# Optimization experiments

Measured on AMD Instinct MI355X. Metric: run time of the kernel, lower is better.

The kernel has to match this reference:

```python
import jax, jax.numpy as jnp
import numpy as np

B, S, D, H, O = 256, 64, 256, 1024, 512
N_CELLS = 3


def setup_inputs() -> dict:
    key = jax.random.key(0)
    ks = jax.random.split(key, 16)

    def u(k, shape, fan):
        return (jax.random.uniform(k, shape, jnp.float32, -1.0, 1.0) / np.float32(np.sqrt(fan)))

    inp = {"inputs": jax.random.normal(ks[0], (B, S, D), jnp.float32)}
    in_dims = [D, H, H]
    i = 1
    for c in range(N_CELLS):
        inp[f"w_ih_{c}"] = u(ks[i], (3 * H, in_dims[c]), H); i += 1
        inp[f"w_hh_{c}"] = u(ks[i], (3 * H, H), H); i += 1
        inp[f"b_ih_{c}"] = u(ks[i], (3 * H,), H); i += 1
        inp[f"b_hh_{c}"] = u(ks[i], (3 * H,), H); i += 1
    inp["lin_w"] = u(ks[13], (S, H, O), H)   # per-step linear weights (same_linear=False)
    inp["lin_b"] = u(ks[14], (S, O), H)
    return inp


def _gru_cell(x, h, w_ih, w_hh, b_ih, b_hh):
    # PyTorch GRUCell gate order: r, z, n
    gi = x @ w_ih.T + b_ih          # [B, 3H]
    gh = h @ w_hh.T + b_hh          # [B, 3H]
    i_r, i_z, i_n = jnp.split(gi, 3, axis=-1)
    h_r, h_z, h_n = jnp.split(gh, 3, axis=-1)
    r = jax.nn.sigmoid(i_r + h_r)
    z = jax.nn.sigmoid(i_z + h_z)
    n = jnp.tanh(i_n + r * h_n)
    return (1.0 - z) * n + z * h


def reference(inputs, w_ih_0, w_hh_0, b_ih_0, b_hh_0,
              w_ih_1, w_hh_1, b_ih_1, b_hh_1,
              w_ih_2, w_hh_2, b_ih_2, b_hh_2,
              lin_w, lin_b):
    params = [(w_ih_0, w_hh_0, b_ih_0, b_hh_0),
              (w_ih_1, w_hh_1, b_ih_1, b_hh_1),
              (w_ih_2, w_hh_2, b_ih_2, b_hh_2)]
    batch = inputs.shape[0]
    hdim = w_hh_0.shape[1]

    def step(hs, xs):
        x_t, wL, bL = xs              # [B,D], [H,O], [O]
        new_hs = []
        cur = x_t
        for i, (wi, wh, bi, bh) in enumerate(params):
            h = _gru_cell(cur, hs[i], wi, wh, bi, bh)
            new_hs.append(h)
            cur = h
        out = cur @ wL + bL           # [B,O]
        return tuple(new_hs), out

    h0 = tuple(jnp.zeros((batch, hdim), inputs.dtype) for _ in range(N_CELLS))
    xs = (jnp.swapaxes(inputs, 0, 1), lin_w, lin_b)  # scan over seq dim
    hs, outs = jax.lax.scan(step, h0, xs)            # outs: [S,B,O]
    return (jnp.swapaxes(outs, 0, 1), hs[0], hs[1], hs[2])
```

## Files before the change

kernel.cpp:

```cpp
#include <hip/hip_runtime.h>
#include <hip/hip_bf16.h>
#include <stdint.h>

#define B_ 256
#define S_ 64
#define D_ 256
#define H_ 1024
#define O_ 512
#define G_ 3072
#define BH_ (B_ * H_)
#define RING_ 32

typedef unsigned short u16;
typedef __attribute__((ext_vector_type(8))) short bf16x8;
typedef __attribute__((ext_vector_type(4))) float f32x4;

#define MFMA16(a, b, c) __builtin_amdgcn_mfma_f32_16x16x32_bf16((a), (b), (c), 0, 0, 0)

__device__ __forceinline__ u16 f2b(float f) {
    union { float f; uint32_t u; } v; v.f = f;
    uint32_t u = v.u;
    return (u16)((u + 0x7fffu + ((u >> 16) & 1u)) >> 16);
}

__device__ __forceinline__ void gl_lds16(const u16* g, u16* l) {
    __builtin_amdgcn_global_load_lds(
        (const __attribute__((address_space(1))) unsigned int*)g,
        (__attribute__((address_space(3))) unsigned int*)l, 16, 0, 0);
}
__device__ __forceinline__ unsigned long long gld_sys(const u16* p) {
    unsigned long long v;
    asm volatile("global_load_dwordx2 %0, %1, off sc0 sc1"
                 : "=v"(v) : "v"(p) : "memory");
    return v;
}
__device__ __forceinline__ void gst_sys(u16* p, unsigned long long v) {
    asm volatile("global_store_dwordx2 %0, %1, off sc0 sc1"
                 :: "v"(p), "v"(v) : "memory");
}
__device__ __forceinline__ void waitflag(int* f, int n) {
    while (__hip_atomic_load(f, __ATOMIC_RELAXED, __HIP_MEMORY_SCOPE_SYSTEM) < n)
        __builtin_amdgcn_s_sleep(8);
    asm volatile("" ::: "memory");
}
__device__ __forceinline__ void postflag(int* f) {
    __hip_atomic_fetch_add(f, 1, __ATOMIC_RELAXED, __HIP_MEMORY_SCOPE_SYSTEM);
}


__global__ void k_conv(const float* __restrict__ s, u16* __restrict__ d, int n4) {
    int i = blockIdx.x * blockDim.x + threadIdx.x;
    int st = gridDim.x * blockDim.x;
    for (; i < n4; i += st) {
        float4 v = ((const float4*)s)[i];
        ushort4 o;
        o.x = f2b(v.x); o.y = f2b(v.y); o.z = f2b(v.z); o.w = f2b(v.w);
        ((ushort4*)d)[i] = o;
    }
}

__global__ __launch_bounds__(256) void k_twl(const float* __restrict__ w, u16* __restrict__ o) {
    __shared__ float tile[32][33];
    int bid = blockIdx.x;
    int t = bid >> 9;
    int rem = bid & 511;
    int j0 = (rem >> 4) << 5;
    int o0 = (rem & 15) << 5;
    int tx = threadIdx.x & 31, ty = threadIdx.x >> 5;
    const float* base = w + (size_t)t * (H_ * O_);
#pragma unroll
    for (int i = 0; i < 4; ++i) {
        int r = ty + (i << 3);
        tile[r][tx] = base[(size_t)(j0 + r) * O_ + o0 + tx];
    }
    __syncthreads();
    u16* ob = o + (size_t)t * (O_ * H_);
#pragma unroll
    for (int i = 0; i < 4; ++i) {
        int r = ty + (i << 3);
        ob[(size_t)(o0 + r) * H_ + j0 + tx] = f2b(tile[tx][r]);
    }
}


struct GruArgs {
    const u16* Xb;
    const u16 *Wi0, *Wh0, *Wi1, *Wh1, *Wi2, *Wh2;
    const float *bi0, *bh0, *bi1, *bh1, *bi2, *bh2;
    u16 *h0, *h1, *h2a;
    const u16* WLt;
    const float* lb;
    float* out;
    int* ready;
    int* consumed;
};

__global__ __launch_bounds__(512, 1) void k_gru(GruArgs p) {
    __shared__ u16 Wb[3][3][128 * 64];
    __shared__ u16 Ab[2][32 * 64];

    const int w = blockIdx.x;
    const int xcd = w & 7;
    const int slot = w >> 3;
    const int role = slot >> 3;
    const int sub = slot & 7;
    const int b0 = sub * 32;

    const int tid = threadIdx.x;
    const int wid = tid >> 6, lane = tid & 63;
    const int fr = lane & 15, kc = lane >> 4;

    const int arow = tid >> 4;
    const int acol = (tid & 15) << 2;
    const int adst = arow * 64 + ((((tid & 15) >> 1) ^ (arow & 7)) << 3) + ((tid & 1) << 2);

    int sw0 = ((kc ^ (fr & 7)) << 3);
    int sw1 = (((4 + kc) ^ (fr & 7)) << 3);

    int* ready = p.ready;
    int* consumed = p.consumed;

    if (role < 3) {
        const u16 *Wi, *Wh; const float *bi, *bh; int K0;
        if (role == 0)      { Wi = p.Wi0; Wh = p.Wh0; bi = p.bi0; bh = p.bh0; K0 = D_; }
        else if (role == 1) { Wi = p.Wi1; Wh = p.Wh1; bi = p.bi1; bh = p.bh1; K0 = H_; }
        else                { Wi = p.Wi2; Wh = p.Wh2; bi = p.bi2; bh = p.bh2; K0 = H_; }
        const int nXc = K0 >> 6;
        const int nC = nXc + 16;
        const int j0 = xcd * 128;
        const int jme = j0 + (wid << 4) + fr;
        const float b_r = bi[jme] + bh[jme];
        const float b_z = bi[H_ + jme] + bh[H_ + jme];
        const float b_i = bi[2 * H_ + jme];
        const float b_h = bh[2 * H_ + jme];

        const u16 *A0 = nullptr, *Ah = nullptr; int ld0 = H_;
        u16* hout = nullptr;

        f32x4 hcar[2] = {};

        auto LA = [&](int c) -> unsigned long long {
            const u16* s = (c < nXc) ? (A0 + (size_t)arow * ld0 + (c << 6) + acol)
                                     : (Ah + (size_t)arow * H_ + ((c - nXc) << 6) + acol);
            return gld_sys(s);
        };
        auto SW = [&](int c, int nb) {
            if (c < nXc) {
                int ko = c << 6;
#pragma unroll
                for (int hh = 0; hh < 2; ++hh) {
                    int ci = (hh << 9) + tid, jr = ci >> 3, c8 = ci & 7;
                    size_t ro = (size_t)(j0 + jr) * K0 + ko + ((c8 ^ (jr & 7)) << 3);
                    gl_lds16(Wi + ro,                       &Wb[nb][0][ci << 3]);
                    gl_lds16(Wi + (size_t)H_ * K0 + ro,     &Wb[nb][1][ci << 3]);
                    gl_lds16(Wi + (size_t)2 * H_ * K0 + ro, &Wb[nb][2][ci << 3]);
                }
            } else {
                int ko = (c - nXc) << 6;
#pragma unroll
                for (int hh = 0; hh < 2; ++hh) {
                    int ci = (hh << 9) + tid, jr = ci >> 3, c8 = ci & 7;
                    size_t ro = (size_t)(j0 + jr) * H_ + ko + ((c8 ^ (jr & 7)) << 3);
                    gl_lds16(Wh + ro,                       &Wb[nb][0][ci << 3]);
                    gl_lds16(Wh + (size_t)H_ * H_ + ro,     &Wb[nb][1][ci << 3]);
                    gl_lds16(Wh + (size_t)2 * H_ * H_ + ro, &Wb[nb][2][ci << 3]);
                }
            }
        };

        for (int t = 0; t < S_; ++t) {
            if (role == 0) {
                if (t) waitflag(&ready[0 * 64 + t - 1], 64);
                A0 = p.Xb + (size_t)b0 * (S_ * D_) + t * D_; ld0 = S_ * D_;
                Ah = p.h0 + (size_t)((t + RING_ - 1) & (RING_ - 1)) * BH_ + (size_t)b0 * H_;
                hout = p.h0 + (size_t)(t & (RING_ - 1)) * BH_;
            } else if (role == 1) {
                waitflag(&ready[0 * 64 + t], 64);
                if (t) waitflag(&ready[1 * 64 + t - 1], 64);
                A0 = p.h0 + (size_t)(t & (RING_ - 1)) * BH_ + (size_t)b0 * H_; ld0 = H_;
                Ah = p.h1 + (size_t)((t + RING_ - 1) & (RING_ - 1)) * BH_ + (size_t)b0 * H_;
                hout = p.h1 + (size_t)(t & (RING_ - 1)) * BH_;
            } else {
                waitflag(&ready[1 * 64 + t], 64);
                if (t) waitflag(&ready[2 * 64 + t - 1], 64);
                A0 = p.h1 + (size_t)(t & (RING_ - 1)) * BH_ + (size_t)b0 * H_; ld0 = H_;
                Ah = p.h2a + (size_t)t * BH_ + (size_t)b0 * H_;
                hout = p.h2a + (size_t)(t + 1) * BH_;
            }

            f32x4 accR[2] = {}, accZ[2] = {}, accI[2] = {}, accN[2] = {};

            SW(0, 0);
            unsigned long long la_t = LA(0);
            unsigned long long r1 = LA(1);
            unsigned long long r0 = LA(2);
            SW(1, 1);
            asm volatile("s_waitcnt vmcnt(8)" ::: "memory");
            *(unsigned long long*)&Ab[0][adst] = la_t;
            asm volatile("s_waitcnt lgkmcnt(0)" ::: "memory");
            __builtin_amdgcn_sched_barrier(0);

            auto BODY = [&](int s, unsigned long long& laReg) {
                if (s + 2 < nC) asm volatile("s_waitcnt vmcnt(7)" ::: "memory");
                else            asm volatile("s_waitcnt vmcnt(0)" ::: "memory");
                __builtin_amdgcn_s_barrier();
                __builtin_amdgcn_sched_barrier(0);
                if (s + 1 < nC) *(unsigned long long*)&Ab[(s + 1) & 1][adst] = laReg;
                if (s + 3 < nC) laReg = LA(s + 3);
                if (s + 2 < nC) SW(s + 2, (s + 2) % 3);
                __builtin_amdgcn_sched_barrier(0);
                const int cur = s & 1;
                const int wcur = s % 3;
                const int bo = ((wid << 4) + fr) * 64;
                bf16x8 a00 = *(const bf16x8*)&Ab[cur][fr * 64 + sw0];
                bf16x8 a01 = *(const bf16x8*)&Ab[cur][fr * 64 + sw1];
                bf16x8 a10 = *(const bf16x8*)&Ab[cur][(16 + fr) * 64 + sw0];
                bf16x8 a11 = *(const bf16x8*)&Ab[cur][(16 + fr) * 64 + sw1];
                bf16x8 rr0 = *(const bf16x8*)&Wb[wcur][0][bo + sw0];
                bf16x8 rr1 = *(const bf16x8*)&Wb[wcur][0][bo + sw1];
                bf16x8 zz0 = *(const bf16x8*)&Wb[wcur][1][bo + sw0];
                bf16x8 zz1 = *(const bf16x8*)&Wb[wcur][1][bo + sw1];
                bf16x8 qq0 = *(const bf16x8*)&Wb[wcur][2][bo + sw0];
                bf16x8 qq1 = *(const bf16x8*)&Wb[wcur][2][bo + sw1];
                asm volatile("s_waitcnt lgkmcnt(0)" ::: "memory");
                __builtin_amdgcn_sched_barrier(0);
                __builtin_amdgcn_s_setprio(1);
                accR[0] = MFMA16(a00, rr0, accR[0]); accR[0] = MFMA16(a01, rr1, accR[0]);
                accR[1] = MFMA16(a10, rr0, accR[1]); accR[1] = MFMA16(a11, rr1, accR[1]);
                accZ[0] = MFMA16(a00, zz0, accZ[0]); accZ[0] = MFMA16(a01, zz1, accZ[0]);
                accZ[1] = MFMA16(a10, zz0, accZ[1]); accZ[1] = MFMA16(a11, zz1, accZ[1]);
                if (s < nXc) {
                    accI[0] = MFMA16(a00, qq0, accI[0]); accI[0] = MFMA16(a01, qq1, accI[0]);
                    accI[1] = MFMA16(a10, qq0, accI[1]); accI[1] = MFMA16(a11, qq1, accI[1]);
                } else {
                    accN[0] = MFMA16(a00, qq0, accN[0]); accN[0] = MFMA16(a01, qq1, accN[0]);
                    accN[1] = MFMA16(a10, qq0, accN[1]); accN[1] = MFMA16(a11, qq1, accN[1]);
                }
                __builtin_amdgcn_s_setprio(0);
            };
            for (int s = 0; s < nC; s += 2) { BODY(s, r1); BODY(s + 1, r0); }

            if (role <= 1 && t >= RING_) waitflag(&consumed[role * 64 + (t - RING_)], 128);

            u16* hrep = &Wb[0][0][0];
#pragma unroll
            for (int m = 0; m < 2; ++m)
#pragma unroll
                for (int i = 0; i < 4; ++i) {
                    int row = m * 16 + kc * 4 + i;
                    float rv = 1.f / (1.f + __expf(-(accR[m][i] + b_r)));
                    float zv = 1.f / (1.f + __expf(-(accZ[m][i] + b_z)));
                    float nv = tanhf(accI[m][i] + b_i + rv * (accN[m][i] + b_h));
                    float hn = (1.f - zv) * nv + zv * hcar[m][i];
                    hcar[m][i] = hn;
                    hrep[row * 128 + (wid << 4) + fr] = f2b(hn);
                }
            __syncthreads();
            {
                int rr = tid >> 4, jo = (tid & 15) << 3;
                unsigned long long v0 = *(const unsigned long long*)&hrep[rr * 128 + jo];
                unsigned long long v1 = *(const unsigned long long*)&hrep[rr * 128 + jo + 4];
                u16* dst = hout + (size_t)(b0 + rr) * H_ + j0 + jo;
                gst_sys(dst, v0);
                gst_sys(dst + 4, v1);
            }
            if (t == S_ - 1) {
                float* ob = p.out + (size_t)B_ * S_ * O_ + (size_t)role * BH_;
#pragma unroll
                for (int m = 0; m < 2; ++m)
#pragma unroll
                    for (int i = 0; i < 4; ++i) {
                        int row = m * 16 + kc * 4 + i;
                        ob[(size_t)(b0 + row) * H_ + jme] = hcar[m][i];
                    }
            }
            asm volatile("s_waitcnt vmcnt(0)" ::: "memory");
            __syncthreads();
            if (tid == 0) {
                postflag(&ready[role * 64 + t]);
                if (role == 0) { if (t) postflag(&consumed[0 * 64 + t - 1]); }
                else if (role == 1) {
                    postflag(&consumed[0 * 64 + t]);
                    if (t) postflag(&consumed[1 * 64 + t - 1]);
                } else {
                    postflag(&consumed[1 * 64 + t]);
                }
            }
            __syncthreads();
        }
    } else {
        const int o0 = xcd << 6;
        const int nC = 16;
        const int mg = wid >> 2, og = wid & 3;
        const u16 *A0 = nullptr, *Wl = nullptr;

        auto LAl = [&](int c) -> unsigned long long {
            return gld_sys(A0 + (size_t)arow * H_ + (c << 6) + acol);
        };
        auto SWl = [&](int c, int nb) {
            int orow = tid >> 3, c8 = tid & 7;
            gl_lds16(Wl + (size_t)(o0 + orow) * H_ + (c << 6) + ((c8 ^ (orow & 7)) << 3),
                     &Wb[nb][0][tid << 3]);
        };

        for (int t = 0; t < S_; ++t) {
            waitflag(&ready[2 * 64 + t], 64);
            A0 = p.h2a + (size_t)(t + 1) * BH_ + (size_t)b0 * H_;
            Wl = p.WLt + (size_t)t * (O_ * H_);

            f32x4 acc = {0.f, 0.f, 0.f, 0.f};
            SWl(0, 0);
            unsigned long long la_t = LAl(0);
            unsigned long long r1 = LAl(1);
            unsigned long long r0 = LAl(2);
            SWl(1, 1);
            asm volatile("s_waitcnt vmcnt(3)" ::: "memory");
            *(unsigned long long*)&Ab[0][adst] = la_t;
            asm volatile("s_waitcnt lgkmcnt(0)" ::: "memory");
            __builtin_amdgcn_sched_barrier(0);

            auto BODYL = [&](int s, unsigned long long& laReg) {
                if (s + 2 < nC) asm volatile("s_waitcnt vmcnt(2)" ::: "memory");
                else            asm volatile("s_waitcnt vmcnt(0)" ::: "memory");
                __builtin_amdgcn_s_barrier();
                __builtin_amdgcn_sched_barrier(0);
                if (s + 1 < nC) *(unsigned long long*)&Ab[(s + 1) & 1][adst] = laReg;
                if (s + 3 < nC) laReg = LAl(s + 3);
                if (s + 2 < nC) SWl(s + 2, (s + 2) % 3);
                __builtin_amdgcn_sched_barrier(0);
                const int cur = s & 1;
                const int wcur = s % 3;
                bf16x8 a0 = *(const bf16x8*)&Ab[cur][(mg * 16 + fr) * 64 + sw0];
                bf16x8 a1 = *(const bf16x8*)&Ab[cur][(mg * 16 + fr) * 64 + sw1];
                bf16x8 w0 = *(const bf16x8*)&Wb[wcur][0][(og * 16 + fr) * 64 + sw0];
                bf16x8 w1 = *(const bf16x8*)&Wb[wcur][0][(og * 16 + fr) * 64 + sw1];
                asm volatile("s_waitcnt lgkmcnt(0)" ::: "memory");
                __builtin_amdgcn_sched_barrier(0);
                __builtin_amdgcn_s_setprio(1);
                acc = MFMA16(a0, w0, acc);
                acc = MFMA16(a1, w1, acc);
                __builtin_amdgcn_s_setprio(0);
            };
            for (int s = 0; s < nC; s += 2) { BODYL(s, r1); BODYL(s + 1, r0); }

            float bb = p.lb[t * O_ + o0 + og * 16 + fr];
#pragma unroll
            for (int i = 0; i < 4; ++i) {
                int row = mg * 16 + kc * 4 + i;
                p.out[((size_t)(b0 + row) * S_ + t) * O_ + o0 + og * 16 + fr] = acc[i] + bb;
            }
        }
    }
}


extern "C" void kernel_launch(void* const* d_in, const int* in_sizes, int n_in,
                              void* d_out, int out_size, void* d_ws, size_t ws_size,
                              hipStream_t stream) {
    (void)in_sizes; (void)n_in; (void)out_size; (void)ws_size;
    const float* x   = (const float*)d_in[0];
    const float* wi0 = (const float*)d_in[1];
    const float* wh0 = (const float*)d_in[2];
    const float* bi0 = (const float*)d_in[3];
    const float* bh0 = (const float*)d_in[4];
    const float* wi1 = (const float*)d_in[5];
    const float* wh1 = (const float*)d_in[6];
    const float* bi1 = (const float*)d_in[7];
    const float* bh1 = (const float*)d_in[8];
    const float* wi2 = (const float*)d_in[9];
    const float* wh2 = (const float*)d_in[10];
    const float* bi2 = (const float*)d_in[11];
    const float* bh2 = (const float*)d_in[12];
    const float* lw  = (const float*)d_in[13];
    const float* lb  = (const float*)d_in[14];

    char* base = (char*)d_ws;
    size_t off = 0;
    auto alloc = [&](size_t bytes) {
        char* p = base + off;
        off = (off + bytes + 255) & ~(size_t)255;
        return p;
    };
    u16* Xb  = (u16*)alloc((size_t)B_ * S_ * D_ * 2);
    u16* Wi0 = (u16*)alloc((size_t)G_ * D_ * 2);
    u16* Wh0 = (u16*)alloc((size_t)G_ * H_ * 2);
    u16* Wi1 = (u16*)alloc((size_t)G_ * H_ * 2);
    u16* Wh1 = (u16*)alloc((size_t)G_ * H_ * 2);
    u16* Wi2 = (u16*)alloc((size_t)G_ * H_ * 2);
    u16* Wh2 = (u16*)alloc((size_t)G_ * H_ * 2);
    u16* h0  = (u16*)alloc((size_t)RING_ * BH_ * 2);
    u16* h1  = (u16*)alloc((size_t)RING_ * BH_ * 2);
    u16* h2a = (u16*)alloc((size_t)(S_ + 1) * BH_ * 2);
    u16* WLt = (u16*)alloc((size_t)S_ * O_ * H_ * 2);
    int* flags = (int*)alloc((size_t)(3 * 64 + 2 * 64) * 4);
    int* ready = flags;
    int* consumed = flags + 3 * 64;

    k_conv<<<1024, 256, 0, stream>>>(x,   Xb,  (B_ * S_ * D_) / 4);
    k_conv<<<1024, 256, 0, stream>>>(wi0, Wi0, (G_ * D_) / 4);
    k_conv<<<1024, 256, 0, stream>>>(wh0, Wh0, (G_ * H_) / 4);
    k_conv<<<1024, 256, 0, stream>>>(wi1, Wi1, (G_ * H_) / 4);
    k_conv<<<1024, 256, 0, stream>>>(wh1, Wh1, (G_ * H_) / 4);
    k_conv<<<1024, 256, 0, stream>>>(wi2, Wi2, (G_ * H_) / 4);
    k_conv<<<1024, 256, 0, stream>>>(wh2, Wh2, (G_ * H_) / 4);
    k_twl<<<S_ * 512, 256, 0, stream>>>(lw, WLt);
    hipMemsetAsync(h0 + (size_t)(RING_ - 1) * BH_, 0, (size_t)BH_ * 2, stream);
    hipMemsetAsync(h1 + (size_t)(RING_ - 1) * BH_, 0, (size_t)BH_ * 2, stream);
    hipMemsetAsync(h2a, 0, (size_t)BH_ * 2, stream);
    hipMemsetAsync(flags, 0, (size_t)(3 * 64 + 2 * 64) * 4, stream);

    GruArgs ga;
    ga.Xb = Xb;
    ga.Wi0 = Wi0; ga.Wh0 = Wh0; ga.Wi1 = Wi1; ga.Wh1 = Wh1; ga.Wi2 = Wi2; ga.Wh2 = Wh2;
    ga.bi0 = bi0; ga.bh0 = bh0; ga.bi1 = bi1; ga.bh1 = bh1; ga.bi2 = bi2; ga.bh2 = bh2;
    ga.h0 = h0; ga.h1 = h1; ga.h2a = h2a;
    ga.WLt = WLt; ga.lb = lb; ga.out = (float*)d_out;
    ga.ready = ready; ga.consumed = consumed;

    void* args[] = {&ga};
    hipLaunchCooperativeKernel((void*)k_gru, dim3(256), dim3(512), args, 0, stream);
}
```

Baseline: 2.395 ms.

## Load GRU weights directly into registers instead of staging through LDS

```diff
diff --git a/kernel.cpp b/kernel.cpp
--- a/kernel.cpp
+++ b/kernel.cpp
@@ -23,11 +23,6 @@
     return (u16)((u + 0x7fffu + ((u >> 16) & 1u)) >> 16);
 }
 
-__device__ __forceinline__ void gl_lds16(const u16* g, u16* l) {
-    __builtin_amdgcn_global_load_lds(
-        (const __attribute__((address_space(1))) unsigned int*)g,
-        (__attribute__((address_space(3))) unsigned int*)l, 16, 0, 0);
-}
 __device__ __forceinline__ unsigned long long gld_sys(const u16* p) {
     unsigned long long v;
     asm volatile("global_load_dwordx2 %0, %1, off sc0 sc1"
@@ -95,9 +90,14 @@
     int* consumed;
 };
 
+#define VMW(n)  asm volatile("s_waitcnt vmcnt(" #n ")" ::: "memory")
+#define LGK0    asm volatile("s_waitcnt lgkmcnt(0)" ::: "memory")
+#define SBAR    __builtin_amdgcn_s_barrier()
+#define SCHB    __builtin_amdgcn_sched_barrier(0)
+
 __global__ __launch_bounds__(512, 1) void k_gru(GruArgs p) {
-    __shared__ u16 Wb[3][3][128 * 64];
     __shared__ u16 Ab[2][32 * 64];
+    __shared__ u16 hrep[32 * 128];
 
     const int w = blockIdx.x;
     const int xcd = w & 7;
@@ -114,8 +114,9 @@
     const int acol = (tid & 15) << 2;
     const int adst = arow * 64 + ((((tid & 15) >> 1) ^ (arow & 7)) << 3) + ((tid & 1) << 2);
 
-    int sw0 = ((kc ^ (fr & 7)) << 3);
-    int sw1 = (((4 + kc) ^ (fr & 7)) << 3);
+    const int sw0 = ((kc ^ (fr & 7)) << 3);
+    const int sw1 = (((4 + kc) ^ (fr & 7)) << 3);
+    const int koff = kc << 3;
 
     int* ready = p.ready;
     int* consumed = p.consumed;
@@ -128,11 +129,17 @@
         const int nXc = K0 >> 6;
         const int nC = nXc + 16;
         const int j0 = xcd * 128;
-        const int jme = j0 + (wid << 4) + fr;
+        const int jrow = (wid << 4) + fr;
+        const int jme = j0 + jrow;
         const float b_r = bi[jme] + bh[jme];
         const float b_z = bi[H_ + jme] + bh[H_ + jme];
         const float b_i = bi[2 * H_ + jme];
         const float b_h = bh[2 * H_ + jme];
+
+        const size_t rowX = (size_t)jme * K0;
+        const size_t rowH = (size_t)jme * H_;
+        const size_t gsX = (size_t)H_ * K0;
+        const size_t gsH = (size_t)H_ * H_;
 
         const u16 *A0 = nullptr, *Ah = nullptr; int ld0 = H_;
         u16* hout = nullptr;
@@ -144,29 +151,54 @@
                                      : (Ah + (size_t)arow * H_ + ((c - nXc) << 6) + acol);
             return gld_sys(s);
         };
-        auto SW = [&](int c, int nb) {
-            if (c < nXc) {
-                int ko = c << 6;
-#pragma unroll
-                for (int hh = 0; hh < 2; ++hh) {
-                    int ci = (hh << 9) + tid, jr = ci >> 3, c8 = ci & 7;
-                    size_t ro = (size_t)(j0 + jr) * K0 + ko + ((c8 ^ (jr & 7)) << 3);
-                    gl_lds16(Wi + ro,                       &Wb[nb][0][ci << 3]);
-                    gl_lds16(Wi + (size_t)H_ * K0 + ro,     &Wb[nb][1][ci << 3]);
-                    gl_lds16(Wi + (size_t)2 * H_ * K0 + ro, &Wb[nb][2][ci << 3]);
-                }
-            } else {
-                int ko = (c - nXc) << 6;
-#pragma unroll
-                for (int hh = 0; hh < 2; ++hh) {
-                    int ci = (hh << 9) + tid, jr = ci >> 3, c8 = ci & 7;
-                    size_t ro = (size_t)(j0 + jr) * H_ + ko + ((c8 ^ (jr & 7)) << 3);
-                    gl_lds16(Wh + ro,                       &Wb[nb][0][ci << 3]);
-                    gl_lds16(Wh + (size_t)H_ * H_ + ro,     &Wb[nb][1][ci << 3]);
-                    gl_lds16(Wh + (size_t)2 * H_ * H_ + ro, &Wb[nb][2][ci << 3]);
-                }
-            }
-        };
+
+#define WISS(cc_, W0,W1,W2,W3,W4,W5) do { \
+    int c_ = (cc_); const u16* bx_; size_t gs_; \
+    if (c_ < nXc) { bx_ = Wi + rowX + ((size_t)c_ << 6) + koff; gs_ = gsX; } \
+    else          { bx_ = Wh + rowH + ((size_t)(c_ - nXc) << 6) + koff; gs_ = gsH; } \
+    asm volatile("global_load_dwordx4 %0, %1, off" : "=v"(W0) : "v"(bx_)); \
+    asm volatile("global_load_dwordx4 %0, %1, off" : "=v"(W1) : "v"(bx_ + 32)); \
+    asm volatile("global_load_dwordx4 %0, %1, off" : "=v"(W2) : "v"(bx_ + gs_)); \
+    asm volatile("global_load_dwordx4 %0, %1, off" : "=v"(W3) : "v"(bx_ + gs_ + 32)); \
+    asm volatile("global_load_dwordx4 %0, %1, off" : "=v"(W4) : "v"(bx_ + 2 * gs_)); \
+    asm volatile("global_load_dwordx4 %0, %1, off" : "=v"(W5) : "v"(bx_ + 2 * gs_ + 32)); \
+} while (0)
+
+#define CSTEP(ss_, RING, W0,W1,W2,W3,W4,W5, NIMM) do { \
+    asm volatile("s_waitcnt vmcnt(" #NIMM ")" ::: "memory"); \
+    SBAR; SCHB; \
+    const int s_ = (ss_); const int cur_ = s_ & 1; \
+    if (s_ + 1 < nC) *(unsigned long long*)&Ab[cur_ ^ 1][adst] = RING; \
+    bf16x8 a00 = *(const bf16x8*)&Ab[cur_][fr * 64 + sw0]; \
+    bf16x8 a01 = *(const bf16x8*)&Ab[cur_][fr * 64 + sw1]; \
+    bf16x8 a10 = *(const bf16x8*)&Ab[cur_][(16 + fr) * 64 + sw0]; \
+    bf16x8 a11 = *(const bf16x8*)&Ab[cur_][(16 + fr) * 64 + sw1]; \
+    LGK0; SCHB; \
+    __builtin_amdgcn_s_setprio(1); \
+    { bf16x8 r0_ = *(const bf16x8*)&W0, r1_ = *(const bf16x8*)&W1; \
+      bf16x8 z0_ = *(const bf16x8*)&W2, z1_ = *(const bf16x8*)&W3; \
+      bf16x8 q0_ = *(const bf16x8*)&W4, q1_ = *(const bf16x8*)&W5; \
+      accR[0] = MFMA16(a00, r0_, accR[0]); accR[0] = MFMA16(a01, r1_, accR[0]); \
+      accR[1] = MFMA16(a10, r0_, accR[1]); accR[1] = MFMA16(a11, r1_, accR[1]); \
+      accZ[0] = MFMA16(a00, z0_, accZ[0]); accZ[0] = MFMA16(a01, z1_, accZ[0]); \
+      accZ[1] = MFMA16(a10, z0_, accZ[1]); accZ[1] = MFMA16(a11, z1_, accZ[1]); \
+      if (s_ < nXc) { \
+        accI[0] = MFMA16(a00, q0_, accI[0]); accI[0] = MFMA16(a01, q1_, accI[0]); \
+        accI[1] = MFMA16(a10, q0_, accI[1]); accI[1] = MFMA16(a11, q1_, accI[1]); \
+      } else { \
+        accN[0] = MFMA16(a00, q0_, accN[0]); accN[0] = MFMA16(a01, q1_, accN[0]); \
+        accN[1] = MFMA16(a10, q0_, accN[1]); accN[1] = MFMA16(a11, q1_, accN[1]); \
+      } } \
+    __builtin_amdgcn_s_setprio(0); SCHB; \
+    if (s_ + 5 < nC) RING = LA(s_ + 5); \
+    if (s_ + 4 < nC) WISS(s_ + 4, W0, W1, W2, W3, W4, W5); \
+} while (0)
+
+        uint4 w00, w01, w02, w03, w04, w05;
+        uint4 w10, w11, w12, w13, w14, w15;
+        uint4 w20, w21, w22, w23, w24, w25;
+        uint4 w30, w31, w32, w33, w34, w35;
+        unsigned long long rA0, rA1, rA2, rA3;
 
         for (int t = 0; t < S_; ++t) {
             if (role == 0) {
@@ -190,59 +222,28 @@
 
             f32x4 accR[2] = {}, accZ[2] = {}, accI[2] = {}, accN[2] = {};
 
-            SW(0, 0);
-            unsigned long long la_t = LA(0);
-            unsigned long long r1 = LA(1);
-            unsigned long long r0 = LA(2);
-            SW(1, 1);
-            asm volatile("s_waitcnt vmcnt(8)" ::: "memory");
-            *(unsigned long long*)&Ab[0][adst] = la_t;
-            asm volatile("s_waitcnt lgkmcnt(0)" ::: "memory");
-            __builtin_amdgcn_sched_barrier(0);
-
-            auto BODY = [&](int s, unsigned long long& laReg) {
-                if (s + 2 < nC) asm volatile("s_waitcnt vmcnt(7)" ::: "memory");
-                else            asm volatile("s_waitcnt vmcnt(0)" ::: "memory");
-                __builtin_amdgcn_s_barrier();
-                __builtin_amdgcn_sched_barrier(0);
-                if (s + 1 < nC) *(unsigned long long*)&Ab[(s + 1) & 1][adst] = laReg;
-                if (s + 3 < nC) laReg = LA(s + 3);
-                if (s + 2 < nC) SW(s + 2, (s + 2) % 3);
-                __builtin_amdgcn_sched_barrier(0);
-                const int cur = s & 1;
-                const int wcur = s % 3;
-                const int bo = ((wid << 4) + fr) * 64;
-                bf16x8 a00 = *(const bf16x8*)&Ab[cur][fr * 64 + sw0];
-                bf16x8 a01 = *(const bf16x8*)&Ab[cur][fr * 64 + sw1];
-                bf16x8 a10 = *(const bf16x8*)&Ab[cur][(16 + fr) * 64 + sw0];
-                bf16x8 a11 = *(const bf16x8*)&Ab[cur][(16 + fr) * 64 + sw1];
-                bf16x8 rr0 = *(const bf16x8*)&Wb[wcur][0][bo + sw0];
-                bf16x8 rr1 = *(const bf16x8*)&Wb[wcur][0][bo + sw1];
-                bf16x8 zz0 = *(const bf16x8*)&Wb[wcur][1][bo + sw0];
-                bf16x8 zz1 = *(const bf16x8*)&Wb[wcur][1][bo + sw1];
-                bf16x8 qq0 = *(const bf16x8*)&Wb[wcur][2][bo + sw0];
-                bf16x8 qq1 = *(const bf16x8*)&Wb[wcur][2][bo + sw1];
-                asm volatile("s_waitcnt lgkmcnt(0)" ::: "memory");
-                __builtin_amdgcn_sched_barrier(0);
-                __builtin_amdgcn_s_setprio(1);
-                accR[0] = MFMA16(a00, rr0, accR[0]); accR[0] = MFMA16(a01, rr1, accR[0]);
-                accR[1] = MFMA16(a10, rr0, accR[1]); accR[1] = MFMA16(a11, rr1, accR[1]);
-                accZ[0] = MFMA16(a00, zz0, accZ[0]); accZ[0] = MFMA16(a01, zz1, accZ[0]);
-                accZ[1] = MFMA16(a10, zz0, accZ[1]); accZ[1] = MFMA16(a11, zz1, accZ[1]);
-                if (s < nXc) {
-                    accI[0] = MFMA16(a00, qq0, accI[0]); accI[0] = MFMA16(a01, qq1, accI[0]);
-                    accI[1] = MFMA16(a10, qq0, accI[1]); accI[1] = MFMA16(a11, qq1, accI[1]);
-                } else {
-                    accN[0] = MFMA16(a00, qq0, accN[0]); accN[0] = MFMA16(a01, qq1, accN[0]);
-                    accN[1] = MFMA16(a10, qq0, accN[1]); accN[1] = MFMA16(a11, qq1, accN[1]);
-                }
-                __builtin_amdgcn_s_setprio(0);
-            };
-            for (int s = 0; s < nC; s += 2) { BODY(s, r1); BODY(s + 1, r0); }
+            unsigned long long t0 = LA(0);
+            rA0 = LA(1); WISS(0, w00, w01, w02, w03, w04, w05);
+            rA1 = LA(2); WISS(1, w10, w11, w12, w13, w14, w15);
+            rA2 = LA(3); WISS(2, w20, w21, w22, w23, w24, w25);
+            rA3 = LA(4); WISS(3, w30, w31, w32, w33, w34, w35);
+            VMW(28);
+            *(unsigned long long*)&Ab[0][adst] = t0;
+
+            int s4 = 0;
+            for (; s4 + 7 < nC; s4 += 4) {
+                CSTEP(s4 + 0, rA0, w00, w01, w02, w03, w04, w05, 21);
+                CSTEP(s4 + 1, rA1, w10, w11, w12, w13, w14, w15, 21);
+                CSTEP(s4 + 2, rA2, w20, w21, w22, w23, w24, w25, 21);
+                CSTEP(s4 + 3, rA3, w30, w31, w32, w33, w34, w35, 21);
+            }
+            CSTEP(nC - 4, rA0, w00, w01, w02, w03, w04, w05, 20);
+            CSTEP(nC - 3, rA1, w10, w11, w12, w13, w14, w15, 13);
+            CSTEP(nC - 2, rA2, w20, w21, w22, w23, w24, w25, 6);
+            CSTEP(nC - 1, rA3, w30, w31, w32, w33, w34, w35, 0);
 
             if (role <= 1 && t >= RING_) waitflag(&consumed[role * 64 + (t - RING_)], 128);
 
-            u16* hrep = &Wb[0][0][0];
 #pragma unroll
             for (int m = 0; m < 2; ++m)
 #pragma unroll
@@ -287,21 +288,46 @@
                 }
             }
             __syncthreads();
+            asm volatile("s_waitcnt vmcnt(0) lgkmcnt(0)" ::: "memory");
         }
+#undef CSTEP
+#undef WISS
     } else {
         const int o0 = xcd << 6;
         const int nC = 16;
         const int mg = wid >> 2, og = wid & 3;
+        const size_t rowO = (size_t)(o0 + og * 16 + fr) * H_;
         const u16 *A0 = nullptr, *Wl = nullptr;
 
         auto LAl = [&](int c) -> unsigned long long {
             return gld_sys(A0 + (size_t)arow * H_ + (c << 6) + acol);
         };
-        auto SWl = [&](int c, int nb) {
-            int orow = tid >> 3, c8 = tid & 7;
-            gl_lds16(Wl + (size_t)(o0 + orow) * H_ + (c << 6) + ((c8 ^ (orow & 7)) << 3),
-                     &Wb[nb][0][tid << 3]);
-        };
+
+#define WLISS(cc_, W0, W1) do { int c_ = (cc_); \
+    const u16* bx_ = Wl + rowO + ((size_t)c_ << 6) + koff; \
+    asm volatile("global_load_dwordx4 %0, %1, off" : "=v"(W0) : "v"(bx_)); \
+    asm volatile("global_load_dwordx4 %0, %1, off" : "=v"(W1) : "v"(bx_ + 32)); \
+} while (0)
+
+#define HSTEP(ss_, RING, W0, W1, NIMM) do { \
+    asm volatile("s_waitcnt vmcnt(" #NIMM ")" ::: "memory"); \
+    SBAR; SCHB; \
+    const int s_ = (ss_); const int cur_ = s_ & 1; \
+    if (s_ + 1 < nC) *(unsigned long long*)&Ab[cur_ ^ 1][adst] = RING; \
+    bf16x8 a0 = *(const bf16x8*)&Ab[cur_][(mg * 16 + fr) * 64 + sw0]; \
+    bf16x8 a1 = *(const bf16x8*)&Ab[cur_][(mg * 16 + fr) * 64 + sw1]; \
+    LGK0; SCHB; \
+    __builtin_amdgcn_s_setprio(1); \
+    { bf16x8 w0_ = *(const bf16x8*)&W0, w1_ = *(const bf16x8*)&W1; \
+      acc = MFMA16(a0, w0_, acc); \
+      acc = MFMA16(a1, w1_, acc); } \
+    __builtin_amdgcn_s_setprio(0); SCHB; \
+    if (s_ + 5 < nC) RING = LAl(s_ + 5); \
+    if (s_ + 4 < nC) WLISS(s_ + 4, W0, W1); \
+} while (0)
+
+        uint4 h00, h01, h10, h11, h20, h21, h30, h31;
+        unsigned long long rA0, rA1, rA2, rA3;
 
         for (int t = 0; t < S_; ++t) {
             waitflag(&ready[2 * 64 + t], 64);
@@ -309,39 +335,25 @@
             Wl = p.WLt + (size_t)t * (O_ * H_);
 
             f32x4 acc = {0.f, 0.f, 0.f, 0.f};
-            SWl(0, 0);
-            unsigned long long la_t = LAl(0);
-            unsigned long long r1 = LAl(1);
-            unsigned long long r0 = LAl(2);
-            SWl(1, 1);
-            asm volatile("s_waitcnt vmcnt(3)" ::: "memory");
-            *(unsigned long long*)&Ab[0][adst] = la_t;
-            asm volatile("s_waitcnt lgkmcnt(0)" ::: "memory");
-            __builtin_amdgcn_sched_barrier(0);
-
-            auto BODYL = [&](int s, unsigned long long& laReg) {
-                if (s + 2 < nC) asm volatile("s_waitcnt vmcnt(2)" ::: "memory");
-                else            asm volatile("s_waitcnt vmcnt(0)" ::: "memory");
-                __builtin_amdgcn_s_barrier();
-                __builtin_amdgcn_sched_barrier(0);
-                if (s + 1 < nC) *(unsigned long long*)&Ab[(s + 1) & 1][adst] = laReg;
-                if (s + 3 < nC) laReg = LAl(s + 3);
-                if (s + 2 < nC) SWl(s + 2, (s + 2) % 3);
-                __builtin_amdgcn_sched_barrier(0);
-                const int cur = s & 1;
-                const int wcur = s % 3;
-                bf16x8 a0 = *(const bf16x8*)&Ab[cur][(mg * 16 + fr) * 64 + sw0];
-                bf16x8 a1 = *(const bf16x8*)&Ab[cur][(mg * 16 + fr) * 64 + sw1];
-                bf16x8 w0 = *(const bf16x8*)&Wb[wcur][0][(og * 16 + fr) * 64 + sw0];
-                bf16x8 w1 = *(const bf16x8*)&Wb[wcur][0][(og * 16 + fr) * 64 + sw1];
-                asm volatile("s_waitcnt lgkmcnt(0)" ::: "memory");
-                __builtin_amdgcn_sched_barrier(0);
-                __builtin_amdgcn_s_setprio(1);
-                acc = MFMA16(a0, w0, acc);
-                acc = MFMA16(a1, w1, acc);
-                __builtin_amdgcn_s_setprio(0);
-            };
-            for (int s = 0; s < nC; s += 2) { BODYL(s, r1); BODYL(s + 1, r0); }
+            unsigned long long t0 = LAl(0);
+            rA0 = LAl(1); WLISS(0, h00, h01);
+            rA1 = LAl(2); WLISS(1, h10, h11);
+            rA2 = LAl(3); WLISS(2, h20, h21);
+            rA3 = LAl(4); WLISS(3, h30, h31);
+            VMW(12);
+            *(unsigned long long*)&Ab[0][adst] = t0;
+
+            int s4 = 0;
+            for (; s4 + 7 < nC; s4 += 4) {
+                HSTEP(s4 + 0, rA0, h00, h01, 9);
+                HSTEP(s4 + 1, rA1, h10, h11, 9);
+                HSTEP(s4 + 2, rA2, h20, h21, 9);
+                HSTEP(s4 + 3, rA3, h30, h31, 9);
+            }
+            HSTEP(nC - 4, rA0, h00, h01, 8);
+            HSTEP(nC - 3, rA1, h10, h11, 5);
+            HSTEP(nC - 2, rA2, h20, h21, 2);
+            HSTEP(nC - 1, rA3, h30, h31, 0);
 
             float bb = p.lb[t * O_ + o0 + og * 16 + fr];
 #pragma unroll
@@ -349,7 +361,10 @@
                 int row = mg * 16 + kc * 4 + i;
                 p.out[((size_t)(b0 + row) * S_ + t) * O_ + o0 + og * 16 + fr] = acc[i] + bb;
             }
+            asm volatile("s_waitcnt vmcnt(0) lgkmcnt(0)" ::: "memory");
         }
+#undef HSTEP
+#undef WLISS
     }
 }
 
```

Result: slower. 3.503 ms (+46.3%).

## Restructure GRU chunk pipeline with single barrier per chunk and weight prefetch to LDS trash

Applied to the files above, without the earlier changes.

```diff
diff --git a/kernel.cpp b/kernel.cpp
--- a/kernel.cpp
+++ b/kernel.cpp
@@ -95,9 +95,15 @@
     int* consumed;
 };
 
+#define VMW(n)  asm volatile("s_waitcnt vmcnt(" #n ")" ::: "memory")
+#define LGK0    asm volatile("s_waitcnt lgkmcnt(0)" ::: "memory")
+#define SBAR    __builtin_amdgcn_s_barrier()
+#define SCHB    __builtin_amdgcn_sched_barrier(0)
+
 __global__ __launch_bounds__(512, 1) void k_gru(GruArgs p) {
     __shared__ u16 Wb[3][3][128 * 64];
     __shared__ u16 Ab[2][32 * 64];
+    __shared__ u16 trash[512];
 
     const int w = blockIdx.x;
     const int xcd = w & 7;
@@ -114,8 +120,8 @@
     const int acol = (tid & 15) << 2;
     const int adst = arow * 64 + ((((tid & 15) >> 1) ^ (arow & 7)) << 3) + ((tid & 1) << 2);
 
-    int sw0 = ((kc ^ (fr & 7)) << 3);
-    int sw1 = (((4 + kc) ^ (fr & 7)) << 3);
+    const int sw0 = ((kc ^ (fr & 7)) << 3);
+    const int sw1 = (((4 + kc) ^ (fr & 7)) << 3);
 
     int* ready = p.ready;
     int* consumed = p.consumed;
@@ -167,6 +173,47 @@
                 }
             }
         };
+
+#define CBODY(S_, LAS, LAL, NIMM) do { \
+    const int s_ = (S_); \
+    LGK0; SBAR; \
+    if (s_ + 2 < nC) { LAL = LA(s_ + 2); SW(s_ + 2, (s_ + 2) % 3); } \
+    if (wid == sub && s_ + 4 < nC) { \
+        int v_ = s_ + 4; int gg_ = lane >> 4; if (gg_ > 2) gg_ = 2; \
+        const u16* pb_ = (v_ < nXc) \
+            ? Wi + (size_t)(gg_ * H_ + j0 + sub * 16 + (lane & 15)) * K0 + (v_ << 6) \
+            : Wh + (size_t)(gg_ * H_ + j0 + sub * 16 + (lane & 15)) * H_ + ((v_ - nXc) << 6); \
+        gl_lds16(pb_, trash); \
+    } \
+    VMW(NIMM); SCHB; \
+    if (s_ + 1 < nC) *(unsigned long long*)&Ab[(s_ + 1) & 1][adst] = LAS; \
+    const int cur_ = s_ & 1, wcur_ = s_ % 3; \
+    const int bo_ = ((wid << 4) + fr) * 64; \
+    bf16x8 a00 = *(const bf16x8*)&Ab[cur_][fr * 64 + sw0]; \
+    bf16x8 a01 = *(const bf16x8*)&Ab[cur_][fr * 64 + sw1]; \
+    bf16x8 a10 = *(const bf16x8*)&Ab[cur_][(16 + fr) * 64 + sw0]; \
+    bf16x8 a11 = *(const bf16x8*)&Ab[cur_][(16 + fr) * 64 + sw1]; \
+    bf16x8 rr0 = *(const bf16x8*)&Wb[wcur_][0][bo_ + sw0]; \
+    bf16x8 rr1 = *(const bf16x8*)&Wb[wcur_][0][bo_ + sw1]; \
+    bf16x8 zz0 = *(const bf16x8*)&Wb[wcur_][1][bo_ + sw0]; \
+    bf16x8 zz1 = *(const bf16x8*)&Wb[wcur_][1][bo_ + sw1]; \
+    bf16x8 qq0 = *(const bf16x8*)&Wb[wcur_][2][bo_ + sw0]; \
+    bf16x8 qq1 = *(const bf16x8*)&Wb[wcur_][2][bo_ + sw1]; \
+    LGK0; SCHB; \
+    __builtin_amdgcn_s_setprio(1); \
+    accR[0] = MFMA16(a00, rr0, accR[0]); accR[0] = MFMA16(a01, rr1, accR[0]); \
+    accR[1] = MFMA16(a10, rr0, accR[1]); accR[1] = MFMA16(a11, rr1, accR[1]); \
+    accZ[0] = MFMA16(a00, zz0, accZ[0]); accZ[0] = MFMA16(a01, zz1, accZ[0]); \
+    accZ[1] = MFMA16(a10, zz0, accZ[1]); accZ[1] = MFMA16(a11, zz1, accZ[1]); \
+    if (s_ < nXc) { \
+        accI[0] = MFMA16(a00, qq0, accI[0]); accI[0] = MFMA16(a01, qq1, accI[0]); \
+        accI[1] = MFMA16(a10, qq0, accI[1]); accI[1] = MFMA16(a11, qq1, accI[1]); \
+    } else { \
+        accN[0] = MFMA16(a00, qq0, accN[0]); accN[0] = MFMA16(a01, qq1, accN[0]); \
+        accN[1] = MFMA16(a10, qq0, accN[1]); accN[1] = MFMA16(a11, qq1, accN[1]); \
+    } \
+    __builtin_amdgcn_s_setprio(0); \
+} while (0)
 
         for (int t = 0; t < S_; ++t) {
             if (role == 0) {
@@ -190,55 +237,21 @@
 
             f32x4 accR[2] = {}, accZ[2] = {}, accI[2] = {}, accN[2] = {};
 
+            unsigned long long la0 = LA(0);
             SW(0, 0);
-            unsigned long long la_t = LA(0);
-            unsigned long long r1 = LA(1);
-            unsigned long long r0 = LA(2);
+            unsigned long long la1 = LA(1);
             SW(1, 1);
-            asm volatile("s_waitcnt vmcnt(8)" ::: "memory");
-            *(unsigned long long*)&Ab[0][adst] = la_t;
-            asm volatile("s_waitcnt lgkmcnt(0)" ::: "memory");
-            __builtin_amdgcn_sched_barrier(0);
-
-            auto BODY = [&](int s, unsigned long long& laReg) {
-                if (s + 2 < nC) asm volatile("s_waitcnt vmcnt(7)" ::: "memory");
-                else            asm volatile("s_waitcnt vmcnt(0)" ::: "memory");
-                __builtin_amdgcn_s_barrier();
-                __builtin_amdgcn_sched_barrier(0);
-                if (s + 1 < nC) *(unsigned long long*)&Ab[(s + 1) & 1][adst] = laReg;
-                if (s + 3 < nC) laReg = LA(s + 3);
-                if (s + 2 < nC) SW(s + 2, (s + 2) % 3);
-                __builtin_amdgcn_sched_barrier(0);
-                const int cur = s & 1;
-                const int wcur = s % 3;
-                const int bo = ((wid << 4) + fr) * 64;
-                bf16x8 a00 = *(const bf16x8*)&Ab[cur][fr * 64 + sw0];
-                bf16x8 a01 = *(const bf16x8*)&Ab[cur][fr * 64 + sw1];
-                bf16x8 a10 = *(const bf16x8*)&Ab[cur][(16 + fr) * 64 + sw0];
-                bf16x8 a11 = *(const bf16x8*)&Ab[cur][(16 + fr) * 64 + sw1];
-                bf16x8 rr0 = *(const bf16x8*)&Wb[wcur][0][bo + sw0];
-                bf16x8 rr1 = *(const bf16x8*)&Wb[wcur][0][bo + sw1];
-                bf16x8 zz0 = *(const bf16x8*)&Wb[wcur][1][bo + sw0];
-                bf16x8 zz1 = *(const bf16x8*)&Wb[wcur][1][bo + sw1];
-                bf16x8 qq0 = *(const bf16x8*)&Wb[wcur][2][bo + sw0];
-                bf16x8 qq1 = *(const bf16x8*)&Wb[wcur][2][bo + sw1];
-                asm volatile("s_waitcnt lgkmcnt(0)" ::: "memory");
-                __builtin_amdgcn_sched_barrier(0);
-                __builtin_amdgcn_s_setprio(1);
-                accR[0] = MFMA16(a00, rr0, accR[0]); accR[0] = MFMA16(a01, rr1, accR[0]);
-                accR[1] = MFMA16(a10, rr0, accR[1]); accR[1] = MFMA16(a11, rr1, accR[1]);
-                accZ[0] = MFMA16(a00, zz0, accZ[0]); accZ[0] = MFMA16(a01, zz1, accZ[0]);
-                accZ[1] = MFMA16(a10, zz0, accZ[1]); accZ[1] = MFMA16(a11, zz1, accZ[1]);
-                if (s < nXc) {
-                    accI[0] = MFMA16(a00, qq0, accI[0]); accI[0] = MFMA16(a01, qq1, accI[0]);
-                    accI[1] = MFMA16(a10, qq0, accI[1]); accI[1] = MFMA16(a11, qq1, accI[1]);
-                } else {
-                    accN[0] = MFMA16(a00, qq0, accN[0]); accN[0] = MFMA16(a01, qq1, accN[0]);
-                    accN[1] = MFMA16(a10, qq0, accN[1]); accN[1] = MFMA16(a11, qq1, accN[1]);
-                }
-                __builtin_amdgcn_s_setprio(0);
-            };
-            for (int s = 0; s < nC; s += 2) { BODY(s, r1); BODY(s + 1, r0); }
+            VMW(13);
+            *(unsigned long long*)&Ab[0][adst] = la0;
+
+            for (int s = 0; s + 4 < nC; s += 2) {
+                CBODY(s,     la1, la0, 13);
+                CBODY(s + 1, la0, la1, 13);
+            }
+            CBODY(nC - 4, la1, la0, 13);
+            CBODY(nC - 3, la0, la1, 13);
+            CBODY(nC - 2, la1, la0, 6);
+            CBODY(nC - 1, la0, la1, 0);
 
             if (role <= 1 && t >= RING_) waitflag(&consumed[role * 64 + (t - RING_)], 128);
 
@@ -287,7 +300,9 @@
                 }
             }
             __syncthreads();
+            asm volatile("s_waitcnt vmcnt(0) lgkmcnt(0)" ::: "memory");
         }
+#undef CBODY
     } else {
         const int o0 = xcd << 6;
         const int nC = 16;
@@ -317,17 +332,17 @@
             asm volatile("s_waitcnt vmcnt(3)" ::: "memory");
             *(unsigned long long*)&Ab[0][adst] = la_t;
             asm volatile("s_waitcnt lgkmcnt(0)" ::: "memory");
-            __builtin_amdgcn_sched_barrier(0);
+            SCHB;
 
             auto BODYL = [&](int s, unsigned long long& laReg) {
                 if (s + 2 < nC) asm volatile("s_waitcnt vmcnt(2)" ::: "memory");
                 else            asm volatile("s_waitcnt vmcnt(0)" ::: "memory");
-                __builtin_amdgcn_s_barrier();
-                __builtin_amdgcn_sched_barrier(0);
+                SBAR;
+                SCHB;
                 if (s + 1 < nC) *(unsigned long long*)&Ab[(s + 1) & 1][adst] = laReg;
                 if (s + 3 < nC) laReg = LAl(s + 3);
                 if (s + 2 < nC) SWl(s + 2, (s + 2) % 3);
-                __builtin_amdgcn_sched_barrier(0);
+                SCHB;
                 const int cur = s & 1;
                 const int wcur = s % 3;
                 bf16x8 a0 = *(const bf16x8*)&Ab[cur][(mg * 16 + fr) * 64 + sw0];
@@ -335,7 +350,7 @@
                 bf16x8 w0 = *(const bf16x8*)&Wb[wcur][0][(og * 16 + fr) * 64 + sw0];
                 bf16x8 w1 = *(const bf16x8*)&Wb[wcur][0][(og * 16 + fr) * 64 + sw1];
                 asm volatile("s_waitcnt lgkmcnt(0)" ::: "memory");
-                __builtin_amdgcn_sched_barrier(0);
+                SCHB;
                 __builtin_amdgcn_s_setprio(1);
                 acc = MFMA16(a0, w0, acc);
                 acc = MFMA16(a1, w1, acc);
@@ -349,6 +364,7 @@
                 int row = mg * 16 + kc * 4 + i;
                 p.out[((size_t)(b0 + row) * S_ + t) * O_ + o0 + og * 16 + fr] = acc[i] + bb;
             }
+            asm volatile("s_waitcnt vmcnt(0) lgkmcnt(0)" ::: "memory");
         }
     }
 }
```

Result: slower. 2.757 ms (+15.1%).
